# Optimization experiments

Hardware: AMD Instinct MI355X
Metric: run time of the kernel (lower is better)

The kernel has to match this reference:

```python
import jax, jax.numpy as jnp
import numpy as np

B, L, D = 2, 2048, 2048
H, KVH, HD = 16, 4, 128
GROUPS = H // KVH  # 4 == KVH (required by this module's v_proj sizing)
EPS = 1e-6
SCALE = HD ** -0.5
NEG = -1e9


def setup_inputs() -> dict:
    key = jax.random.key(0)
    ks = jax.random.split(key, 6)
    hidden_states = jax.random.normal(ks[0], (B, L, D), jnp.float32)
    # RoPE tables (b, l, head_dim), HF-style: angles duplicated across halves
    half = HD // 2
    inv_freq = 1.0 / (1e6 ** (jnp.arange(half, dtype=jnp.float32) / half))
    ang = jnp.arange(L, dtype=jnp.float32)[:, None] * inv_freq[None, :]  # (L, half)
    emb = jnp.concatenate([ang, ang], axis=-1)  # (L, HD)
    cos = jnp.broadcast_to(jnp.cos(emb)[None], (B, L, HD))
    sin = jnp.broadcast_to(jnp.sin(emb)[None], (B, L, HD))
    # additive causal mask (b,1,l,l)
    m = jnp.triu(jnp.full((L, L), NEG, jnp.float32), k=1)
    attention_mask = jnp.broadcast_to(m[None, None], (B, 1, L, L))
    s = 0.02
    wq = jax.random.normal(ks[1], (H * HD, D), jnp.float32) * s
    wk = jax.random.normal(ks[2], (KVH * HD, D), jnp.float32) * s
    wv = jax.random.normal(ks[3], (KVH * HD, D), jnp.float32) * s
    wo = jax.random.normal(ks[4], (D, H * HD), jnp.float32) * s
    q_norm_w = jnp.ones((HD,), jnp.float32)
    k_norm_w = jnp.ones((HD,), jnp.float32)
    return dict(hidden_states=hidden_states, cos=cos, sin=sin,
                attention_mask=attention_mask, wq=wq, wk=wk, wv=wv, wo=wo,
                q_norm_w=q_norm_w, k_norm_w=k_norm_w)


def _rmsnorm(x, w):
    var = jnp.mean(x * x, axis=-1, keepdims=True)
    return w * (x * jax.lax.rsqrt(var + EPS))


def _rotate_half(x):
    u, v = jnp.split(x, 2, axis=-1)
    return jnp.concatenate([-v, u], axis=-1)


def reference(hidden_states, cos, sin, attention_mask, wq, wk, wv, wo, q_norm_w, k_norm_w):
    b, l, _ = hidden_states.shape
    q = (hidden_states @ wq.T).reshape(b, l, H, HD).transpose(0, 2, 1, 3)   # (b,H,l,hd)
    k = (hidden_states @ wk.T).reshape(b, l, KVH, HD).transpose(0, 2, 1, 3)
    v = (hidden_states @ wv.T).reshape(b, l, KVH, HD).transpose(0, 2, 1, 3)
    q = _rmsnorm(q, q_norm_w)
    k = _rmsnorm(k, k_norm_w)
    c = cos[:, None]  # (b,1,l,hd)
    s = sin[:, None]
    q = q * c + _rotate_half(q) * s
    k = k * c + _rotate_half(k) * s
    # GQA: repeat each kv head GROUPS times consecutively (matches repeat_n)
    k = jnp.repeat(k, GROUPS, axis=1)
    v = jnp.repeat(v, GROUPS, axis=1)
    attn = jnp.einsum('bhqd,bhkd->bhqk', q, k) * SCALE + attention_mask
    attn = jax.nn.softmax(attn, axis=-1)
    out = jnp.einsum('bhqk,bhkd->bhqd', attn, v)
    out = out.transpose(0, 2, 1, 3).reshape(b, l, H * HD)
    return out @ wo.T
```

## Files before the change

### kernel.cpp

```cpp
#include <hip/hip_runtime.h>


#define SEQL 2048
#define DMODEL 2048
#define NH 16
#define NKVH 4
#define HDIM 128
#define SCALE_QK 0.08838834764831845f
#define LOG2E 1.4426950408889634f
#define INFF 3.0e38f

typedef __attribute__((ext_vector_type(8))) short bf16x8;
typedef __attribute__((ext_vector_type(4))) float f32x4;
typedef __attribute__((ext_vector_type(4))) unsigned int u32x4;

__device__ __forceinline__ unsigned short f2bf(float x) {
  union { float f; unsigned u; } v; v.f = x;
  unsigned r = v.u + 0x7fffu + ((v.u >> 16) & 1u);
  return (unsigned short)(r >> 16);
}
__device__ __forceinline__ float bf2f(unsigned short u) {
  union { unsigned u; float f; } v; v.u = ((unsigned)u) << 16;
  return v.f;
}

__global__ __launch_bounds__(256) void cast_kernel(const float* __restrict__ src,
                                                   unsigned short* __restrict__ dst,
                                                   int n8) {
  int i = blockIdx.x * 256 + threadIdx.x;
  if (i >= n8) return;
  const f32x4* s4 = (const f32x4*)src;
  f32x4 a = s4[2 * i], b = s4[2 * i + 1];
  union { unsigned short s[8]; u32x4 v; } o;
  o.s[0] = f2bf(a[0]); o.s[1] = f2bf(a[1]); o.s[2] = f2bf(a[2]); o.s[3] = f2bf(a[3]);
  o.s[4] = f2bf(b[0]); o.s[5] = f2bf(b[1]); o.s[6] = f2bf(b[2]); o.s[7] = f2bf(b[3]);
  ((u32x4*)dst)[i] = o.v;
}

__global__ __launch_bounds__(256) void cast3_kernel(const float* __restrict__ s0,
                                                    const float* __restrict__ s1,
                                                    const float* __restrict__ s2,
                                                    unsigned short* __restrict__ dst,
                                                    int n0, int n1, int n2) {
  int i = blockIdx.x * 256 + threadIdx.x;
  const float* src;
  int j;
  if (i < n0) { src = s0; j = i; }
  else if (i < n0 + n1) { src = s1; j = i - n0; }
  else if (i < n0 + n1 + n2) { src = s2; j = i - n0 - n1; }
  else return;
  const f32x4* s4 = (const f32x4*)src;
  f32x4 a = s4[2 * j], b = s4[2 * j + 1];
  union { unsigned short s[8]; u32x4 v; } o;
  o.s[0] = f2bf(a[0]); o.s[1] = f2bf(a[1]); o.s[2] = f2bf(a[2]); o.s[3] = f2bf(a[3]);
  o.s[4] = f2bf(b[0]); o.s[5] = f2bf(b[1]); o.s[6] = f2bf(b[2]); o.s[7] = f2bf(b[3]);
  ((u32x4*)dst)[i] = o.v;
}

template <int OUT_BF16>
__global__ __launch_bounds__(512) void gemm_bt(const unsigned short* __restrict__ A,
                                               const unsigned short* __restrict__ B,
                                               void* __restrict__ C,
                                               int M, int N, int K) {
  __shared__ unsigned short As[128 * 64];
  __shared__ unsigned short Bs[128 * 64];
  int tid = threadIdx.x;
  int w = tid >> 6, lane = tid & 63;
  int lr = lane & 15, lg = lane >> 4;
  int nx = N >> 7;
  int lid = (int)blockIdx.x + (int)blockIdx.y * nx;
  int chunk = nx >> 3;
  int xcd = lid & 7;
  int local = lid >> 3;
  int bx = chunk * xcd + local % chunk;
  int by = local / chunk;
  int m0 = by * 128, n0 = bx * 128;
  int wr = (w >> 2) * 64, wc = (w & 3) * 32;
  f32x4 zero4 = {0.f, 0.f, 0.f, 0.f};
  f32x4 acc[4][2];
  for (int i = 0; i < 4; ++i)
    for (int j = 0; j < 2; ++j) acc[i][j] = zero4;

  for (int k0 = 0; k0 < K; k0 += 64) {
    __syncthreads();
    for (int i = 0; i < 2; ++i) {
      int o = i * 8192 + tid * 16;
      int row = o >> 7, cb = o & 127;
      int scb = cb ^ ((row & 7) << 4);
      const char* ga = (const char*)(A + (size_t)(m0 + row) * K + k0) + scb;
      const char* gb = (const char*)(B + (size_t)(n0 + row) * K + k0) + scb;
      __builtin_amdgcn_global_load_lds(
          (const __attribute__((address_space(1))) void*)ga,
          (__attribute__((address_space(3))) void*)((char*)As + i * 8192 + w * 1024),
          16, 0, 0);
      __builtin_amdgcn_global_load_lds(
          (const __attribute__((address_space(1))) void*)gb,
          (__attribute__((address_space(3))) void*)((char*)Bs + i * 8192 + w * 1024),
          16, 0, 0);
    }
    asm volatile("s_waitcnt vmcnt(0)" ::: "memory");
    __syncthreads();

    for (int kk = 0; kk < 2; ++kk) {
      bf16x8 a[4], b[2];
      for (int i = 0; i < 4; ++i) {
        int row = wr + i * 16 + lr;
        int col = kk * 64 + lg * 16;
        a[i] = *(const bf16x8*)((const char*)As + row * 128 + (col ^ ((row & 7) << 4)));
      }
      for (int j = 0; j < 2; ++j) {
        int row = wc + j * 16 + lr;
        int col = kk * 64 + lg * 16;
        b[j] = *(const bf16x8*)((const char*)Bs + row * 128 + (col ^ ((row & 7) << 4)));
      }
      for (int i = 0; i < 4; ++i)
        for (int j = 0; j < 2; ++j)
          acc[i][j] = __builtin_amdgcn_mfma_f32_16x16x32_bf16(a[i], b[j], acc[i][j], 0, 0, 0);
    }
  }

  for (int i = 0; i < 4; ++i)
    for (int j = 0; j < 2; ++j) {
      int row = m0 + wr + i * 16 + lg * 4;
      int col = n0 + wc + j * 16 + lr;
      for (int r = 0; r < 4; ++r) {
        if (OUT_BF16)
          ((unsigned short*)C)[(size_t)(row + r) * N + col] = f2bf(acc[i][j][r]);
        else
          ((float*)C)[(size_t)(row + r) * N + col] = acc[i][j][r];
      }
    }
}

__global__ __launch_bounds__(64) void prep_kernel(const unsigned short* __restrict__ qkv,
                                                  const float* __restrict__ cosb,
                                                  const float* __restrict__ sinb,
                                                  const float* __restrict__ qw,
                                                  const float* __restrict__ kw,
                                                  unsigned short* __restrict__ Qb,
                                                  unsigned short* __restrict__ Kb,
                                                  unsigned short* __restrict__ Vtb)
{
  int l = blockIdx.x, b = blockIdx.y, d = threadIdx.x;
  size_t row = (size_t)b * SEQL + l;
  const unsigned short* src = qkv + row * 3072;
  float c0 = cosb[row * HDIM + d], c1 = cosb[row * HDIM + d + 64];
  float s0 = sinb[row * HDIM + d], s1 = sinb[row * HDIM + d + 64];
  float qw0 = qw[d], qw1 = qw[d + 64];
  float kw0 = kw[d], kw1 = kw[d + 64];
  const float qscale = SCALE_QK * LOG2E;

  float x0[20], x1[20], ss[20];
#pragma unroll
  for (int h = 0; h < 20; ++h) {
    x0[h] = bf2f(src[h * HDIM + d]);
    x1[h] = bf2f(src[h * HDIM + d + 64]);
    ss[h] = x0[h] * x0[h] + x1[h] * x1[h];
  }
#pragma unroll
  for (int m = 1; m < 64; m <<= 1) {
#pragma unroll
    for (int h = 0; h < 20; ++h) ss[h] += __shfl_xor(ss[h], m);
  }
#pragma unroll
  for (int h = 0; h < 16; ++h) {
    float inv = rsqrtf(ss[h] * (1.0f / 128.0f) + 1e-6f);
    float n0 = x0[h] * inv * qw0, n1 = x1[h] * inv * qw1;
    float r0 = (n0 * c0 - n1 * s0) * qscale;
    float r1 = (n1 * c1 + n0 * s1) * qscale;
    unsigned short* dst = Qb + (((size_t)(b * NH + h)) * SEQL + l) * HDIM;
    dst[d] = f2bf(r0);
    dst[d + 64] = f2bf(r1);
  }
#pragma unroll
  for (int h = 0; h < 4; ++h) {
    float inv = rsqrtf(ss[16 + h] * (1.0f / 128.0f) + 1e-6f);
    float n0 = x0[16 + h] * inv * kw0, n1 = x1[16 + h] * inv * kw1;
    float r0 = n0 * c0 - n1 * s0;
    float r1 = n1 * c1 + n0 * s1;
    unsigned short* dst = Kb + (((size_t)(b * NKVH + h)) * SEQL + l) * HDIM;
    dst[d] = f2bf(r0);
    dst[d + 64] = f2bf(r1);
  }
  int lt = l & 31, lb = l & ~31;
  int lp = lb + 2 * (lt & 15) + (lt >> 4);
#pragma unroll
  for (int h = 0; h < NKVH; ++h) {
    unsigned short v0 = src[2560 + h * HDIM + d];
    unsigned short v1 = src[2560 + h * HDIM + d + 64];
    unsigned short* dst = Vtb + ((size_t)(b * NKVH + h) * HDIM) * SEQL;
    dst[(size_t)d * SEQL + lp] = v0;
    dst[(size_t)(d + 64) * SEQL + lp] = v1;
  }
}

__global__ __launch_bounds__(512) void flash_kernel(const unsigned short* __restrict__ Qb,
                                                    const unsigned short* __restrict__ Kb,
                                                    const unsigned short* __restrict__ Vtb,
                                                    unsigned short* __restrict__ AOb)
{
  __shared__ unsigned short Ks[2][32 * 128];
  __shared__ unsigned short Vs[2][128 * 32];
  __shared__ unsigned short Ps[128 * 32];

  int tid = threadIdx.x, w = tid >> 6, lane = tid & 63;
  int lr = lane & 15, lg = lane >> 4;
  int lid = (int)blockIdx.x + ((int)blockIdx.y << 4);
  int work = ((lid & 7) << 6) | (lid >> 3);
  int bh = work >> 4;
  int xi = work & 15;
  int qt = ((work >> 5) & 1) ? 15 - xi : xi;
  int b = bh >> 4, h = bh & 15, hk = h >> 2;
  int q0 = qt * 128;
  int qrow_base = 16 * w + lg * 4;

  const unsigned short* Qg =
      Qb + (((size_t)(b * NH + h)) * SEQL + q0 + 16 * w + lr) * HDIM + lg * 8;
  bf16x8 aq[4];
  for (int kk = 0; kk < 4; ++kk) aq[kk] = *(const bf16x8*)(Qg + kk * 32);

  const unsigned short* Kg0 = Kb + ((size_t)(b * NKVH + hk)) * SEQL * HDIM;
  const unsigned short* Vg0 = Vtb + ((size_t)(b * NKVH + hk)) * HDIM * SEQL;

  float m_run[4], l_part[4];
  f32x4 zero4 = {0.f, 0.f, 0.f, 0.f};
  f32x4 o_acc[8];
  for (int r = 0; r < 4; ++r) { m_run[r] = -INFF; l_part[r] = 0.f; }
  for (int f = 0; f < 8; ++f) o_acc[f] = zero4;

  int nt = 4 * (qt + 1);

  u32x4 kr, vr;

  auto load_tile = [&](int tt) {
    int k0n = tt * 32;
    int o = tid * 16;
    kr = *(const u32x4*)((const char*)Kg0 + (size_t)(k0n + (o >> 8)) * 256 + (o & 255));
    vr = *(const u32x4*)((const char*)Vg0 +
                         (size_t)(o >> 6) * (SEQL * 2) + (size_t)k0n * 2 + (o & 63));
  };
  auto stage_tile = [&](char* kb, char* vb) {
    int o = tid * 16;
    int krow = o >> 8;
    *(u32x4*)(kb + (o ^ ((krow & 7) << 4))) = kr;
    int vrow = o >> 6;
    *(u32x4*)(vb + (o ^ ((vrow & 7) << 4))) = vr;
  };
  auto compute_tile = [&](int t, const char* kb, const char* vb) {
    int k0 = t * 32;
    if (k0 > q0 + 16 * w + 15) return;
    bool needmask = (k0 + 31 > q0 + 16 * w);

    f32x4 s[2];
    for (int j = 0; j < 2; ++j) s[j] = zero4;
    __builtin_amdgcn_s_setprio(1);
    for (int kk = 0; kk < 4; ++kk)
      for (int j = 0; j < 2; ++j) {
        int row = j * 16 + lr;
        bf16x8 bk = *(const bf16x8*)(kb +
                     ((row * 256 + kk * 64 + lg * 16) ^ ((lr & 7) << 4)));
        s[j] = __builtin_amdgcn_mfma_f32_16x16x32_bf16(aq[kk], bk, s[j], 0, 0, 0);
      }
    __builtin_amdgcn_s_setprio(0);

    float v0a[4], v1a[4], mxl[4];
    float gmax = -INFF;
    for (int r = 0; r < 4; ++r) {
      if (needmask) {
        int qg = q0 + qrow_base + r;
        v0a[r] = (k0 + lr <= qg) ? s[0][r] : -INFF;
        v1a[r] = (k0 + 16 + lr <= qg) ? s[1][r] : -INFF;
      } else {
        v0a[r] = s[0][r];
        v1a[r] = s[1][r];
      }
      mxl[r] = fmaxf(v0a[r], v1a[r]);
      gmax = fmaxf(gmax, mxl[r] - m_run[r]);
    }
    if (!__all(gmax <= 8.f)) {
      for (int r = 0; r < 4; ++r) {
        float mx = mxl[r];
        mx = fmaxf(mx, __shfl_xor(mx, 1));
        mx = fmaxf(mx, __shfl_xor(mx, 2));
        mx = fmaxf(mx, __shfl_xor(mx, 4));
        mx = fmaxf(mx, __shfl_xor(mx, 8));
        float m_new = fmaxf(m_run[r], mx);
        float sc = __builtin_amdgcn_exp2f(m_run[r] - m_new);
        l_part[r] *= sc;
        for (int f = 0; f < 8; ++f) o_acc[f][r] *= sc;
        m_run[r] = m_new;
      }
    }
    for (int r = 0; r < 4; ++r) {
      int qrow = qrow_base + r;
      float m_use = m_run[r];
      float p0 = __builtin_amdgcn_exp2f(v0a[r] - m_use);
      float p1 = __builtin_amdgcn_exp2f(v1a[r] - m_use);
      union { float f; unsigned u; } u0, u1;
      u0.f = p0; u1.f = p1;
      *(unsigned int*)((char*)Ps +
          ((qrow * 64 + lr * 4) ^ ((qrow & 7) << 4))) =
          (u0.u >> 16) | (u1.u & 0xFFFF0000u);
      l_part[r] += p0 + p1;
    }

    __builtin_amdgcn_s_setprio(1);
    {
      int prow = 16 * w + lr;
      bf16x8 ap = *(const bf16x8*)((const char*)Ps +
                   ((prow * 64 + lg * 16) ^ ((prow & 7) << 4)));
      for (int f = 0; f < 8; ++f) {
        int vrow = f * 16 + lr;
        bf16x8 bv = *(const bf16x8*)(vb +
                     ((vrow * 64 + lg * 16) ^ ((vrow & 7) << 4)));
        o_acc[f] = __builtin_amdgcn_mfma_f32_16x16x32_bf16(ap, bv, o_acc[f], 0, 0, 0);
      }
    }
    __builtin_amdgcn_s_setprio(0);
  };

  load_tile(0);
  stage_tile((char*)Ks[0], (char*)Vs[0]);
  if (nt > 1) load_tile(1);
  asm volatile("s_waitcnt lgkmcnt(0)" ::: "memory");
  __builtin_amdgcn_s_barrier();
  __builtin_amdgcn_sched_barrier(0);

  for (int t = 0; t < nt; t += 2) {
    if (t + 1 < nt) stage_tile((char*)Ks[1], (char*)Vs[1]);
    if (t + 2 < nt) load_tile(t + 2);
    compute_tile(t, (const char*)Ks[0], (const char*)Vs[0]);
    asm volatile("s_waitcnt lgkmcnt(0)" ::: "memory");
    __builtin_amdgcn_s_barrier();
    __builtin_amdgcn_sched_barrier(0);
    if (t + 1 >= nt) break;
    if (t + 2 < nt) stage_tile((char*)Ks[0], (char*)Vs[0]);
    if (t + 3 < nt) load_tile(t + 3);
    compute_tile(t + 1, (const char*)Ks[1], (const char*)Vs[1]);
    asm volatile("s_waitcnt lgkmcnt(0)" ::: "memory");
    __builtin_amdgcn_s_barrier();
    __builtin_amdgcn_sched_barrier(0);
  }

  unsigned short* dst = AOb + ((size_t)b * SEQL + q0) * DMODEL + h * HDIM;
  for (int r = 0; r < 4; ++r) {
    float l = l_part[r];
    l += __shfl_xor(l, 1);
    l += __shfl_xor(l, 2);
    l += __shfl_xor(l, 4);
    l += __shfl_xor(l, 8);
    float inv = 1.0f / l;
    for (int f = 0; f < 8; ++f)
      dst[(size_t)(qrow_base + r) * DMODEL + f * 16 + lr] = f2bf(o_acc[f][r] * inv);
  }
}

extern "C" void kernel_launch(void* const* d_in, const int* in_sizes, int n_in,
                              void* d_out, int out_size, void* d_ws, size_t ws_size,
                              hipStream_t stream) {
  const float* hidden = (const float*)d_in[0];
  const float* cosb = (const float*)d_in[1];
  const float* sinb = (const float*)d_in[2];
  const float* wq = (const float*)d_in[4];
  const float* wk = (const float*)d_in[5];
  const float* wv = (const float*)d_in[6];
  const float* wo = (const float*)d_in[7];
  const float* qw = (const float*)d_in[8];
  const float* kw = (const float*)d_in[9];
  float* out = (float*)d_out;

  char* ws = (char*)d_ws;
  unsigned short* Xb    = (unsigned short*)(ws + 0);
  unsigned short* Wqkvb = (unsigned short*)(ws + 16777216);
  unsigned short* QKVb  = (unsigned short*)(ws + 29360128);
  unsigned short* Qbuf  = (unsigned short*)(ws + 54525952);
  unsigned short* Kbuf  = (unsigned short*)(ws + 71303168);
  unsigned short* Vtb   = (unsigned short*)(ws + 75497472);
  unsigned short* AOb   = Xb;
  unsigned short* Wob   = QKVb;

  cast_kernel<<<(8388608 / 8 + 255) / 256, 256, 0, stream>>>(hidden, Xb, 8388608 / 8);
  cast3_kernel<<<(786432 + 255) / 256, 256, 0, stream>>>(wq, wk, wv, Wqkvb,
                                                         524288, 131072, 131072);

  gemm_bt<1><<<dim3(3072 / 128, 4096 / 128), 512, 0, stream>>>(Xb, Wqkvb, QKVb, 4096, 3072, 2048);

  prep_kernel<<<dim3(SEQL, 2), 64, 0, stream>>>(QKVb, cosb, sinb, qw, kw, Qbuf, Kbuf, Vtb);

  cast_kernel<<<(4194304 / 8 + 255) / 256, 256, 0, stream>>>(wo, Wob, 4194304 / 8);

  flash_kernel<<<dim3(SEQL / 128, 2 * NH), 512, 0, stream>>>(Qbuf, Kbuf, Vtb, AOb);

  gemm_bt<0><<<dim3(2048 / 128, 4096 / 128), 512, 0, stream>>>(AOb, Wob, out, 4096, 2048, 2048);
}
```

Before: 197.8 us.

## Fuse QK RMSNorm, RoPE and V transpose into QKV projection GEMM epilogue

The QKV projection GEMM now stages its 128x128 output tile in shared memory as bf16, then applies per-head RMSNorm and RoPE (for Q and K heads) or the V transpose directly in the epilogue. This removes the separate prep kernel and the intermediate QKV buffer round-trip through global memory. The price is a longer GEMM epilogue with shuffle reductions and scattered V-transpose stores. The workspace layout is rearranged so Wo no longer aliases the dropped buffer.

Measured after the change: 236.9 us. 1.2x slower.

```diff
diff --git a/kernel.cpp b/kernel.cpp
--- a/kernel.cpp
+++ b/kernel.cpp
@@ -57,10 +57,149 @@
   ((u32x4*)dst)[i] = o.v;
 }
 
-template <int OUT_BF16>
-__global__ __launch_bounds__(512) void gemm_bt(const unsigned short* __restrict__ A,
+__global__ __launch_bounds__(512) void gemm_qkv_fused(
+    const unsigned short* __restrict__ A,
+    const unsigned short* __restrict__ B,
+    const float* __restrict__ cosb,
+    const float* __restrict__ sinb,
+    const float* __restrict__ qw,
+    const float* __restrict__ kw,
+    unsigned short* __restrict__ Qb,
+    unsigned short* __restrict__ Kb,
+    unsigned short* __restrict__ Vtb) {
+  __shared__ unsigned short S[128 * 128];
+  unsigned short* As = S;
+  unsigned short* Bs = S + 128 * 64;
+  const int K = DMODEL, N = 3072;
+  int tid = threadIdx.x;
+  int w = tid >> 6, lane = tid & 63;
+  int lr = lane & 15, lg = lane >> 4;
+  int lid = (int)blockIdx.x + (int)blockIdx.y * 24;
+  int xcd = lid & 7;
+  int local = lid >> 3;
+  int bx = 3 * xcd + local % 3;
+  int by = local / 3;
+  int m0 = by * 128, n0 = bx * 128;
+  int wr = (w >> 2) * 64, wc = (w & 3) * 32;
+  f32x4 zero4 = {0.f, 0.f, 0.f, 0.f};
+  f32x4 acc[4][2];
+  for (int i = 0; i < 4; ++i)
+    for (int j = 0; j < 2; ++j) acc[i][j] = zero4;
+
+  for (int k0 = 0; k0 < K; k0 += 64) {
+    __syncthreads();
+    for (int i = 0; i < 2; ++i) {
+      int o = i * 8192 + tid * 16;
+      int row = o >> 7, cb = o & 127;
+      int scb = cb ^ ((row & 7) << 4);
+      const char* ga = (const char*)(A + (size_t)(m0 + row) * K + k0) + scb;
+      const char* gb = (const char*)(B + (size_t)(n0 + row) * K + k0) + scb;
+      __builtin_amdgcn_global_load_lds(
+          (const __attribute__((address_space(1))) void*)ga,
+          (__attribute__((address_space(3))) void*)((char*)As + i * 8192 + w * 1024),
+          16, 0, 0);
+      __builtin_amdgcn_global_load_lds(
+          (const __attribute__((address_space(1))) void*)gb,
+          (__attribute__((address_space(3))) void*)((char*)Bs + i * 8192 + w * 1024),
+          16, 0, 0);
+    }
+    asm volatile("s_waitcnt vmcnt(0)" ::: "memory");
+    __syncthreads();
+
+    for (int kk = 0; kk < 2; ++kk) {
+      bf16x8 a[4], b[2];
+      for (int i = 0; i < 4; ++i) {
+        int row = wr + i * 16 + lr;
+        int col = kk * 64 + lg * 16;
+        a[i] = *(const bf16x8*)((const char*)As + row * 128 + (col ^ ((row & 7) << 4)));
+      }
+      for (int j = 0; j < 2; ++j) {
+        int row = wc + j * 16 + lr;
+        int col = kk * 64 + lg * 16;
+        b[j] = *(const bf16x8*)((const char*)Bs + row * 128 + (col ^ ((row & 7) << 4)));
+      }
+      for (int i = 0; i < 4; ++i)
+        for (int j = 0; j < 2; ++j)
+          acc[i][j] = __builtin_amdgcn_mfma_f32_16x16x32_bf16(a[i], b[j], acc[i][j], 0, 0, 0);
+    }
+  }
+
+  __syncthreads();
+  for (int i = 0; i < 4; ++i)
+    for (int j = 0; j < 2; ++j) {
+      int rl = wr + i * 16 + lg * 4;
+      int cl = wc + j * 16 + lr;
+      for (int r = 0; r < 4; ++r)
+        S[(rl + r) * 128 + cl] = f2bf(acc[i][j][r]);
+    }
+  __syncthreads();
+
+  int head = bx;
+  int b_ = m0 >> 11;
+  int d = lane;
+  float w0 = 0.f, w1 = 0.f;
+  if (head < 16)      { w0 = qw[d]; w1 = qw[d + 64]; }
+  else if (head < 20) { w0 = kw[d]; w1 = kw[d + 64]; }
+  const float qscale = SCALE_QK * LOG2E;
+
+  for (int c4 = 0; c4 < 4; ++c4) {
+    if (head < 20) {
+      float x0[4], x1[4], ss[4];
+#pragma unroll
+      for (int rr = 0; rr < 4; ++rr) {
+        int rl = 16 * w + c4 * 4 + rr;
+        x0[rr] = bf2f(S[rl * 128 + d]);
+        x1[rr] = bf2f(S[rl * 128 + d + 64]);
+        ss[rr] = x0[rr] * x0[rr] + x1[rr] * x1[rr];
+      }
+#pragma unroll
+      for (int m = 1; m < 64; m <<= 1) {
+#pragma unroll
+        for (int rr = 0; rr < 4; ++rr) ss[rr] += __shfl_xor(ss[rr], m);
+      }
+#pragma unroll
+      for (int rr = 0; rr < 4; ++rr) {
+        int rl = 16 * w + c4 * 4 + rr;
+        int row = m0 + rl;
+        size_t crow = (size_t)row * HDIM;
+        float c0 = cosb[crow + d], c1 = cosb[crow + d + 64];
+        float s0 = sinb[crow + d], s1 = sinb[crow + d + 64];
+        float inv = rsqrtf(ss[rr] * (1.0f / 128.0f) + 1e-6f);
+        float n0v = x0[rr] * inv * w0, n1v = x1[rr] * inv * w1;
+        float r0 = n0v * c0 - n1v * s0;
+        float r1 = n1v * c1 + n0v * s1;
+        int l = row & 2047;
+        if (head < 16) {
+          unsigned short* dst = Qb + (((size_t)(b_ * NH + head)) * SEQL + l) * HDIM;
+          dst[d] = f2bf(r0 * qscale);
+          dst[d + 64] = f2bf(r1 * qscale);
+        } else {
+          unsigned short* dst = Kb + (((size_t)(b_ * NKVH + head - 16)) * SEQL + l) * HDIM;
+          dst[d] = f2bf(r0);
+          dst[d + 64] = f2bf(r1);
+        }
+      }
+    } else {
+#pragma unroll
+      for (int rr = 0; rr < 4; ++rr) {
+        int rl = 16 * w + c4 * 4 + rr;
+        int row = m0 + rl;
+        int l = row & 2047;
+        int lt = l & 31, lb = l & ~31;
+        int lp = lb + 2 * (lt & 15) + (lt >> 4);
+        unsigned short v0 = S[rl * 128 + d];
+        unsigned short v1 = S[rl * 128 + d + 64];
+        unsigned short* dst = Vtb + ((size_t)(b_ * NKVH + head - 20) * HDIM) * SEQL;
+        dst[(size_t)d * SEQL + lp] = v0;
+        dst[(size_t)(d + 64) * SEQL + lp] = v1;
+      }
+    }
+  }
+}
+
+__global__ __launch_bounds__(512) void gemm_wo(const unsigned short* __restrict__ A,
                                                const unsigned short* __restrict__ B,
-                                               void* __restrict__ C,
+                                               float* __restrict__ C,
                                                int M, int N, int K) {
   __shared__ unsigned short As[128 * 64];
   __shared__ unsigned short Bs[128 * 64];
@@ -123,75 +262,9 @@
     for (int j = 0; j < 2; ++j) {
       int row = m0 + wr + i * 16 + lg * 4;
       int col = n0 + wc + j * 16 + lr;
-      for (int r = 0; r < 4; ++r) {
-        if (OUT_BF16)
-          ((unsigned short*)C)[(size_t)(row + r) * N + col] = f2bf(acc[i][j][r]);
-        else
-          ((float*)C)[(size_t)(row + r) * N + col] = acc[i][j][r];
-      }
-    }
-}
-
-__global__ __launch_bounds__(64) void prep_kernel(const unsigned short* __restrict__ qkv,
-                                                  const float* __restrict__ cosb,
-                                                  const float* __restrict__ sinb,
-                                                  const float* __restrict__ qw,
-                                                  const float* __restrict__ kw,
-                                                  unsigned short* __restrict__ Qb,
-                                                  unsigned short* __restrict__ Kb,
-                                                  unsigned short* __restrict__ Vtb)
-{
-  int l = blockIdx.x, b = blockIdx.y, d = threadIdx.x;
-  size_t row = (size_t)b * SEQL + l;
-  const unsigned short* src = qkv + row * 3072;
-  float c0 = cosb[row * HDIM + d], c1 = cosb[row * HDIM + d + 64];
-  float s0 = sinb[row * HDIM + d], s1 = sinb[row * HDIM + d + 64];
-  float qw0 = qw[d], qw1 = qw[d + 64];
-  float kw0 = kw[d], kw1 = kw[d + 64];
-  const float qscale = SCALE_QK * LOG2E;
-
-  float x0[20], x1[20], ss[20];
-#pragma unroll
-  for (int h = 0; h < 20; ++h) {
-    x0[h] = bf2f(src[h * HDIM + d]);
-    x1[h] = bf2f(src[h * HDIM + d + 64]);
-    ss[h] = x0[h] * x0[h] + x1[h] * x1[h];
-  }
-#pragma unroll
-  for (int m = 1; m < 64; m <<= 1) {
-#pragma unroll
-    for (int h = 0; h < 20; ++h) ss[h] += __shfl_xor(ss[h], m);
-  }
-#pragma unroll
-  for (int h = 0; h < 16; ++h) {
-    float inv = rsqrtf(ss[h] * (1.0f / 128.0f) + 1e-6f);
-    float n0 = x0[h] * inv * qw0, n1 = x1[h] * inv * qw1;
-    float r0 = (n0 * c0 - n1 * s0) * qscale;
-    float r1 = (n1 * c1 + n0 * s1) * qscale;
-    unsigned short* dst = Qb + (((size_t)(b * NH + h)) * SEQL + l) * HDIM;
-    dst[d] = f2bf(r0);
-    dst[d + 64] = f2bf(r1);
-  }
-#pragma unroll
-  for (int h = 0; h < 4; ++h) {
-    float inv = rsqrtf(ss[16 + h] * (1.0f / 128.0f) + 1e-6f);
-    float n0 = x0[16 + h] * inv * kw0, n1 = x1[16 + h] * inv * kw1;
-    float r0 = n0 * c0 - n1 * s0;
-    float r1 = n1 * c1 + n0 * s1;
-    unsigned short* dst = Kb + (((size_t)(b * NKVH + h)) * SEQL + l) * HDIM;
-    dst[d] = f2bf(r0);
-    dst[d + 64] = f2bf(r1);
-  }
-  int lt = l & 31, lb = l & ~31;
-  int lp = lb + 2 * (lt & 15) + (lt >> 4);
-#pragma unroll
-  for (int h = 0; h < NKVH; ++h) {
-    unsigned short v0 = src[2560 + h * HDIM + d];
-    unsigned short v1 = src[2560 + h * HDIM + d + 64];
-    unsigned short* dst = Vtb + ((size_t)(b * NKVH + h) * HDIM) * SEQL;
-    dst[(size_t)d * SEQL + lp] = v0;
-    dst[(size_t)(d + 64) * SEQL + lp] = v1;
-  }
+      for (int r = 0; r < 4; ++r)
+        C[(size_t)(row + r) * N + col] = acc[i][j][r];
+    }
 }
 
 __global__ __launch_bounds__(512) void flash_kernel(const unsigned short* __restrict__ Qb,
@@ -372,24 +445,21 @@
   char* ws = (char*)d_ws;
   unsigned short* Xb    = (unsigned short*)(ws + 0);
   unsigned short* Wqkvb = (unsigned short*)(ws + 16777216);
-  unsigned short* QKVb  = (unsigned short*)(ws + 29360128);
-  unsigned short* Qbuf  = (unsigned short*)(ws + 54525952);
-  unsigned short* Kbuf  = (unsigned short*)(ws + 71303168);
-  unsigned short* Vtb   = (unsigned short*)(ws + 75497472);
+  unsigned short* Qbuf  = (unsigned short*)(ws + 29360128);
+  unsigned short* Kbuf  = (unsigned short*)(ws + 46137344);
+  unsigned short* Vtb   = (unsigned short*)(ws + 50331648);
+  unsigned short* Wob   = (unsigned short*)(ws + 54525952);
   unsigned short* AOb   = Xb;
-  unsigned short* Wob   = QKVb;
 
   cast_kernel<<<(8388608 / 8 + 255) / 256, 256, 0, stream>>>(hidden, Xb, 8388608 / 8);
   cast3_kernel<<<(786432 + 255) / 256, 256, 0, stream>>>(wq, wk, wv, Wqkvb,
                                                          524288, 131072, 131072);
-
-  gemm_bt<1><<<dim3(3072 / 128, 4096 / 128), 512, 0, stream>>>(Xb, Wqkvb, QKVb, 4096, 3072, 2048);
-
-  prep_kernel<<<dim3(SEQL, 2), 64, 0, stream>>>(QKVb, cosb, sinb, qw, kw, Qbuf, Kbuf, Vtb);
-
   cast_kernel<<<(4194304 / 8 + 255) / 256, 256, 0, stream>>>(wo, Wob, 4194304 / 8);
 
+  gemm_qkv_fused<<<dim3(24, 32), 512, 0, stream>>>(Xb, Wqkvb, cosb, sinb, qw, kw,
+                                                   Qbuf, Kbuf, Vtb);
+
   flash_kernel<<<dim3(SEQL / 128, 2 * NH), 512, 0, stream>>>(Qbuf, Kbuf, Vtb, AOb);
 
-  gemm_bt<0><<<dim3(2048 / 128, 4096 / 128), 512, 0, stream>>>(AOb, Wob, out, 4096, 2048, 2048);
-}
+  gemm_wo<<<dim3(2048 / 128, 4096 / 128), 512, 0, stream>>>(AOb, Wob, out, 4096, 2048, 2048);
+}
```
